# Kernel optimization log

Measured on AMD Instinct MI355X. Metric: run time of the kernel, lower is better.

Reference implementation:

```python
import jax, jax.numpy as jnp
import numpy as np

NUM_ENT = 50000
DIM = 128
NUM_REL = 1000  # num_rel * 2 (inverse relations)
E = 300000
SLOPE = 0.2      # args.leaky_relu_w
BN_EPS = 1e-5


def _leaky(x):
    return jax.nn.leaky_relu(x, SLOPE)


def _l2norm(x):
    n = jnp.linalg.norm(x, axis=-1, keepdims=True)
    return x / jnp.maximum(n, 1e-12)


def _batchnorm(x):
    # BatchNorm1d, training mode, fresh gamma=1/beta=0
    m = x.mean(axis=0)
    v = x.var(axis=0)
    return (x - m) / jnp.sqrt(v + BN_EPS)


def _propagate(i, j, etype, rel, x, watt, aatt, gcn, norm, num_ent):
    # gather -> relation-aware transform (opn='mult') -> attention -> scatter-add
    trans = x[j] * rel[etype]                       # [E, D]
    comb = jnp.concatenate([x[i], trans], axis=1)   # [E, 2D]
    score = (_leaky(comb @ watt) @ aatt)[:, 0]      # [E]
    # scatter softmax of attention score over destination nodes
    m = jax.ops.segment_max(score, i, num_segments=num_ent)
    m = jnp.where(jnp.isfinite(m), m, 0.0)
    e = jnp.exp(score - m[i])
    s = jax.ops.segment_sum(e, i, num_segments=num_ent)
    alpha = e / (s[i] + 1e-16)
    msg = (trans @ gcn) * alpha[:, None]
    if norm is not None:
        msg = msg * norm[:, None]
    return jax.ops.segment_sum(msg, i, num_segments=num_ent)


def _conv(ent, rel_in, edge_index, edge_type, w1, w2, gcn, loop_rel, watt, aatt):
    # RelationalAwareLayer.forward
    num_ent = ent.shape[0]
    rel = jnp.concatenate([rel_in, loop_rel], axis=0)
    rel = _leaky(rel @ w1) @ w2
    row, col = edge_index[0], edge_index[1]
    deg = jax.ops.segment_sum(jnp.ones((row.shape[0],), jnp.float32), row, num_segments=num_ent)
    dinv = jnp.where(deg > 0, deg ** -0.5, 0.0)
    norm = dinv[row]
    msg_n = _propagate(row, col, edge_type, rel, ent, watt, aatt, gcn, norm, num_ent)
    idx = jnp.arange(num_ent)
    loop_t = jnp.full((num_ent,), rel.shape[0] - 1)
    msg_s = _propagate(idx, idx, loop_t, rel, ent, watt, aatt, gcn, None, num_ent)
    return jnp.tanh(_batchnorm((msg_n + msg_s) / 2.0))


def setup_inputs() -> dict:
    key = jax.random.key(0)
    ks = jax.random.split(key, 24)
    g = lambda k, s: jax.random.normal(k, s, dtype=jnp.float32) * 0.05
    return {
        'edge_index': jax.random.randint(ks[0], (2, E), 0, NUM_ENT),
        'edge_type': jax.random.randint(ks[1], (E,), 0, NUM_REL),
        'ent_info_att': g(ks[2], (NUM_ENT, DIM)),
        'ent_completion_att': g(ks[3], (NUM_ENT, DIM)),
        'rel_completion_att': g(ks[4], (NUM_REL, DIM)),
        'rel_info_att': g(ks[5], (NUM_REL, DIM)),
        'align_linear1_1': g(ks[6], (2 * DIM, DIM)),
        'align_linear1_2': g(ks[7], (DIM, DIM)),
        'align_linear2_1': g(ks[8], (2 * DIM, DIM)),
        'align_linear2_2': g(ks[9], (DIM, DIM)),
        'rel_linear11': g(ks[10], (DIM, DIM)),
        'rel_linear12': g(ks[11], (DIM, DIM)),
        'rel_linear11_align': g(ks[12], (DIM, DIM)),
        'rel_linear12_align': g(ks[13], (DIM, DIM)),
        'all_linear_comp': g(ks[14], (3 * DIM, DIM)),
        # stacked per-layer conv params: [conv1_align, conv1_completion, conv2_align]
        'conv_w1': g(ks[15], (3, DIM, DIM)),
        'conv_w2': g(ks[16], (3, DIM, DIM)),
        'conv_gcn': g(ks[17], (3, DIM, DIM)),
        'conv_loop': g(ks[18], (3, 1, DIM)),
        'conv_watt': g(ks[19], (3, 2 * DIM, DIM)),
        'conv_aatt': g(ks[20], (3, DIM, 1)),
    }


def reference(edge_index, edge_type, ent_info_att, ent_completion_att,
              rel_completion_att, rel_info_att,
              align_linear1_1, align_linear1_2, align_linear2_1, align_linear2_2,
              rel_linear11, rel_linear12, rel_linear11_align, rel_linear12_align,
              all_linear_comp, conv_w1, conv_w2, conv_gcn, conv_loop, conv_watt, conv_aatt):
    # forward_base with num_gcn_layer == 2, dropout rate 0 (identity)
    init_comp = _l2norm(ent_completion_att)
    e1 = _leaky(jnp.concatenate([init_comp, ent_info_att], axis=1) @ align_linear1_1) @ align_linear1_2
    ao1 = _conv(e1, rel_info_att, edge_index, edge_type,
                conv_w1[0], conv_w2[0], conv_gcn[0], conv_loop[0], conv_watt[0], conv_aatt[0])
    co1 = _conv(ent_completion_att, rel_completion_att, edge_index, edge_type,
                conv_w1[1], conv_w2[1], conv_gcn[1], conv_loop[1], conv_watt[1], conv_aatt[1])
    pos1n = _l2norm(co1)
    e2 = _leaky(jnp.concatenate([pos1n, ao1], axis=1) @ align_linear2_1) @ align_linear2_2
    pr1 = _leaky(rel_completion_att @ rel_linear11) @ rel_linear12
    ari = _leaky(rel_info_att @ rel_linear11_align) @ rel_linear12_align
    ao2 = _conv(e2, ari, edge_index, edge_type,
                conv_w1[2], conv_w2[2], conv_gcn[2], conv_loop[2], conv_watt[2], conv_aatt[2])
    out = jnp.concatenate([e1, ao1, ao2], axis=1) @ all_linear_comp
    return (out, co1, pr1)
```

## Files before the change

### kernel.cpp

```cpp
#include <hip/hip_runtime.h>
#include <hip/hip_bf16.h>
#include <math.h>

#define D 128
#define DD 16384
#define NEMAX 96
typedef unsigned short u16;
typedef __attribute__((ext_vector_type(8))) short short8v;
typedef __attribute__((ext_vector_type(4))) short short4v;
typedef __attribute__((ext_vector_type(4))) float f32x4;

__device__ __forceinline__ u16 f2s(float v){
    union { __hip_bfloat16 h; u16 u; } c; c.h = __float2bfloat16(v); return c.u;
}
__device__ __forceinline__ float s2f(u16 u){
    union { __hip_bfloat16 h; u16 u; } c; c.u = u; return __bfloat162float(c.h);
}
__device__ __forceinline__ float lrelu(float x){ return x > 0.f ? x : 0.2f*x; }

__global__ void k_prepz(int* __restrict__ zz, int zw, int* __restrict__ nstart,
                        int* __restrict__ nend, int nb){
    int i = blockIdx.x*blockDim.x + threadIdx.x;
    int stride = gridDim.x*blockDim.x;
    for (int k = i; k < zw; k += stride) zz[k] = 0;
    for (int k = i; k < nb; k += stride){ nstart[k] = 0x7fffffff; nend[k] = -1; }
}
__global__ void k_f2b4(const float* __restrict__ in, u16* __restrict__ out, int n4){
    for (int i = blockIdx.x*blockDim.x + threadIdx.x; i < n4; i += gridDim.x*blockDim.x){
        float4 a = ((const float4*)in)[i];
        short4v pk;
        pk[0] = (short)f2s(a.x); pk[1] = (short)f2s(a.y);
        pk[2] = (short)f2s(a.z); pk[3] = (short)f2s(a.w);
        *(short4v*)(out + (size_t)i*4) = pk;
    }
}
__global__ void k_ideg(const int* __restrict__ row, int* __restrict__ deg, int E_){
    for (int i = blockIdx.x*blockDim.x + threadIdx.x; i < E_; i += gridDim.x*blockDim.x)
        atomicAdd(&deg[row[i]], 1);
}
__global__ void k_scan1(const int* __restrict__ ideg, int* __restrict__ rowptr,
                        int* __restrict__ bsum, int n){
    __shared__ int buf[256];
    int t = threadIdx.x, i = blockIdx.x*256 + t;
    int v = (i < n) ? ideg[i] : 0;
    buf[t] = v;
    __syncthreads();
    #pragma unroll
    for (int o = 1; o < 256; o <<= 1){
        int u = (t >= o) ? buf[t-o] : 0;
        __syncthreads();
        buf[t] += u;
        __syncthreads();
    }
    if (i < n) rowptr[i] = buf[t] - v;
    if (t == 255) bsum[blockIdx.x] = buf[255];
}
__global__ void k_scan2(int* __restrict__ bsum, int nb){
    __shared__ int buf[256];
    __shared__ int carry_s;
    int t = threadIdx.x;
    if (t == 0) carry_s = 0;
    __syncthreads();
    for (int base = 0; base < nb; base += 256){
        int v = (base + t < nb) ? bsum[base + t] : 0;
        buf[t] = v;
        __syncthreads();
        #pragma unroll
        for (int o = 1; o < 256; o <<= 1){
            int u = (t >= o) ? buf[t-o] : 0;
            __syncthreads();
            buf[t] += u;
            __syncthreads();
        }
        if (base + t < nb) bsum[base + t] = carry_s + buf[t] - v;
        int last = buf[255];
        __syncthreads();
        if (t == 0) carry_s += last;
        __syncthreads();
    }
}
__global__ void k_scan3(int* __restrict__ rowptr, const int* __restrict__ bsum,
                        const int* __restrict__ ideg, int* __restrict__ nstart,
                        int* __restrict__ nend, int n, int E_){
    int i = blockIdx.x*blockDim.x + threadIdx.x;
    if (i < n){
        int rpi = rowptr[i] + bsum[i >> 8];
        rowptr[i] = rpi;
        if (i == 0) rowptr[n] = E_;
        if (ideg[i] > 0){
            int b = rpi >> 6;
            atomicMin(&nstart[b], i);
            atomicMax(&nend[b], i);
        }
    }
}
__global__ void k_scatter(const int* __restrict__ row, const int* __restrict__ col,
                          const int* __restrict__ ety, const int* __restrict__ rowptr,
                          int* __restrict__ cnt, unsigned* __restrict__ jk, int E_){
    for (int e = blockIdx.x*blockDim.x + threadIdx.x; e < E_; e += gridDim.x*blockDim.x){
        int i = row[e];
        int pos = rowptr[i] + atomicAdd(&cnt[i], 1);
        jk[pos] = ((unsigned)col[e] & 0xFFFFu) | ((unsigned)ety[e] << 16);
    }
}
__global__ void k_bnapply(const u16* __restrict__ acc, const float* __restrict__ gp,
                          float inv_ne, int n, u16* __restrict__ dstb,
                          float* __restrict__ dstf){
    int d = threadIdx.x & 127;
    float m = gp[d] * inv_ne;
    float var = gp[128 + d] * inv_ne - m*m;
    float sc = rsqrtf(var + 1e-5f);
    for (int i = blockIdx.x*blockDim.x + threadIdx.x; i < n; i += gridDim.x*blockDim.x){
        float v = s2f(acc[i]) * 0.5f;
        float r = tanhf((v - m) * sc);
        dstb[i] = f2s(r);
        if (dstf) dstf[i] = r;
    }
}
__global__ void k_bnapply2(const u16* __restrict__ acc0, const float* __restrict__ gp0,
                           u16* __restrict__ d0b,
                           const u16* __restrict__ acc1, const float* __restrict__ gp1,
                           u16* __restrict__ d1b, float* __restrict__ d1f,
                           float inv_ne, int n, int gb){
    int pb = blockIdx.x >= gb;
    const u16* acc = pb ? acc1 : acc0;
    const float* gp = pb ? gp1 : gp0;
    u16* db = pb ? d1b : d0b;
    float* df = pb ? d1f : nullptr;
    int b = blockIdx.x - (pb ? gb : 0);
    int d = threadIdx.x & 127;
    float m = gp[d] * inv_ne;
    float var = gp[128 + d] * inv_ne - m*m;
    float sc = rsqrtf(var + 1e-5f);
    for (int i = b*blockDim.x + threadIdx.x; i < n; i += gb*blockDim.x){
        float v = s2f(acc[i]) * 0.5f;
        float r = tanhf((v - m) * sc);
        db[i] = f2s(r);
        if (df) df[i] = r;
    }
}

__global__ void k_relprep(const float* __restrict__ rel_comp, const float* __restrict__ rel_info,
        const float* __restrict__ rl11, const float* __restrict__ rl12,
        const float* __restrict__ rl11a, const float* __restrict__ rl12a,
        const float* __restrict__ cloop, const float* __restrict__ cw1,
        const float* __restrict__ cw2, float* __restrict__ pr1out,
        float* __restrict__ rel2all, int NR){
    int b = blockIdx.x, t = threadIdx.x;
    __shared__ float v[D];
    __shared__ float h[D];
    if (b < NR){
        v[t] = rel_comp[(size_t)b*D + t];
        __syncthreads();
        float a = 0.f;
        #pragma unroll 8
        for (int k = 0; k < D; k++) a += v[k] * rl11[(size_t)k*D + t];
        h[t] = lrelu(a);
        __syncthreads();
        float o = 0.f;
        #pragma unroll 8
        for (int k = 0; k < D; k++) o += h[k] * rl12[(size_t)k*D + t];
        pr1out[(size_t)b*D + t] = o;
        return;
    }
    int bb = b - NR;
    int l = bb / (NR+1), r = bb - l*(NR+1);
    float xv;
    if (r == NR)      xv = cloop[l*D + t];
    else if (l == 1)  xv = rel_comp[(size_t)r*D + t];
    else              xv = rel_info[(size_t)r*D + t];
    v[t] = xv;
    __syncthreads();
    if (l == 2 && r < NR){
        float a = 0.f;
        #pragma unroll 8
        for (int k = 0; k < D; k++) a += v[k] * rl11a[(size_t)k*D + t];
        h[t] = lrelu(a);
        __syncthreads();
        float o = 0.f;
        #pragma unroll 8
        for (int k = 0; k < D; k++) o += h[k] * rl12a[(size_t)k*D + t];
        v[t] = o;
        __syncthreads();
    }
    const float* w1 = cw1 + (size_t)l*DD;
    const float* w2 = cw2 + (size_t)l*DD;
    float a = 0.f;
    #pragma unroll 8
    for (int k = 0; k < D; k++) a += v[k] * w1[(size_t)k*D + t];
    h[t] = lrelu(a);
    __syncthreads();
    float o = 0.f;
    #pragma unroll 8
    for (int k = 0; k < D; k++) o += h[k] * w2[(size_t)k*D + t];
    rel2all[((size_t)l*(NR+1) + r)*D + t] = o;
}

struct TEnt { const float* s; u16* d; int ldd; };
struct TTab { TEnt e[18]; };
__global__ void k_wprep(TTab tab){
    TEnt en = tab.e[blockIdx.x];
    int t = threadIdx.x;
    int n = t >> 1, h = t & 1;
    #pragma unroll
    for (int g = 0; g < 8; ++g){
        int k0 = h*64 + g*8;
        short8v pk;
        #pragma unroll
        for (int q = 0; q < 8; ++q) pk[q] = (short)f2s(en.s[(size_t)(k0+q)*D + n]);
        *(short8v*)(en.d + (size_t)n*en.ldd + k0) = pk;
    }
}

struct Srcs { const void* p0; const void* p1; const void* p2; int f0, f1, f2; };

template<int NSEG, int EPI, bool RSN>
__global__ __launch_bounds__(256) void k_mrow(Srcs S, const u16* __restrict__ WT,
        void* __restrict__ out, int NE_){
    __shared__ __align__(16) short As[128*128];
    int tid = threadIdx.x;
    int row0 = blockIdx.x * 128;
    int lane = tid & 63, w = tid >> 6;
    int l15 = lane & 15, lq = lane >> 4;
    int nhalf = w & 1, mquad = w >> 1;
    f32x4 acc[4][4];
    #pragma unroll
    for (int a = 0; a < 4; a++)
        #pragma unroll
        for (int b = 0; b < 4; b++) acc[a][b] = (f32x4){0.f,0.f,0.f,0.f};

    int sr = tid >> 1, sh = tid & 1;
    int rr = row0 + sr; if (rr >= NE_) rr = NE_ - 1;

    #pragma unroll
    for (int s = 0; s < NSEG; ++s){
        const void* sp = (s == 0) ? S.p0 : (s == 1) ? S.p1 : S.p2;
        int sf = (s == 0) ? S.f0 : (s == 1) ? S.f1 : S.f2;
        if (s) __syncthreads();
        #pragma unroll
        for (int g = 0; g < 8; ++g){
            int k8 = sh*64 + g*8;
            short8v pk;
            if (sf){
                const float* fp = (const float*)sp + (size_t)rr*D + k8;
                #pragma unroll
                for (int q = 0; q < 8; ++q) pk[q] = (short)f2s(fp[q]);
            } else {
                pk = *(const short8v*)((const u16*)sp + (size_t)rr*D + k8);
            }
            *(short8v*)(As + sr*D + (((k8>>3) ^ (sr&7))<<3)) = pk;
        }
        if (RSN && s == 0){
            float ss = 0.f;
            #pragma unroll
            for (int g = 0; g < 8; ++g){
                int k8 = sh*64 + g*8;
                short8v v = *(const short8v*)(As + sr*D + (((k8>>3) ^ (sr&7))<<3));
                #pragma unroll
                for (int q = 0; q < 8; ++q){ float f = s2f((u16)v[q]); ss += f*f; }
            }
            ss += __shfl_xor(ss, 1, 64);
            float rsc = 1.f / fmaxf(sqrtf(ss), 1e-12f);
            #pragma unroll
            for (int g = 0; g < 8; ++g){
                int k8 = sh*64 + g*8;
                short* ap = As + sr*D + (((k8>>3) ^ (sr&7))<<3);
                short8v v = *(const short8v*)ap;
                short8v pk;
                #pragma unroll
                for (int q = 0; q < 8; ++q) pk[q] = (short)f2s(s2f((u16)v[q]) * rsc);
                *(short8v*)ap = pk;
            }
        }
        __syncthreads();
        short8v bfr[4][4];
        #pragma unroll
        for (int nt = 0; nt < 4; ++nt)
            #pragma unroll
            for (int kk = 0; kk < 4; ++kk){
                size_t idx = (size_t)(nhalf*64 + nt*16 + l15)*(NSEG*D) + (size_t)s*D + kk*32 + lq*8;
                bfr[nt][kk] = *(const short8v*)(WT + idx);
            }
        #pragma unroll
        for (int mt = 0; mt < 4; ++mt){
            int ar = mquad*64 + mt*16 + l15;
            short8v afr[4];
            #pragma unroll
            for (int kk = 0; kk < 4; ++kk)
                afr[kk] = *(const short8v*)(As + ar*D + (((kk*4 + lq) ^ (ar&7))<<3));
            #pragma unroll
            for (int nt = 0; nt < 4; ++nt)
                #pragma unroll
                for (int kk = 0; kk < 4; ++kk)
                    acc[mt][nt] = __builtin_amdgcn_mfma_f32_16x16x32_bf16(
                        afr[kk], bfr[nt][kk], acc[mt][nt], 0, 0, 0);
        }
    }
    #pragma unroll
    for (int mt = 0; mt < 4; ++mt){
        #pragma unroll
        for (int nt = 0; nt < 4; ++nt){
            #pragma unroll
            for (int r = 0; r < 4; ++r){
                int gr = row0 + mquad*64 + mt*16 + lq*4 + r;
                if (gr >= NE_) continue;
                int c = nhalf*64 + nt*16 + l15;
                float v = acc[mt][nt][r];
                if (EPI == 0) ((float*)out)[(size_t)gr*D + c] = v;
                else ((u16*)out)[(size_t)gr*D + c] = f2s(EPI == 2 ? lrelu(v) : v);
            }
        }
    }
}

struct ConvP { const u16* x; const u16* WT; u16* out; u16* ub; const float* loop; float* gp; };

template<int MODE>
__global__ __launch_bounds__(256) void k_mrow2(ConvP A, ConvP B, int rb, int NE_){
    __shared__ __align__(16) short As[128*128];
    int pb = blockIdx.x >= rb;
    ConvP P = pb ? B : A;
    int row0 = (blockIdx.x - (pb ? rb : 0)) * 128;
    int tid = threadIdx.x;
    int lane = tid & 63, w = tid >> 6;
    int l15 = lane & 15, lq = lane >> 4;
    int nhalf = w & 1, mquad = w >> 1;
    f32x4 acc[4][4];
    #pragma unroll
    for (int a = 0; a < 4; a++)
        #pragma unroll
        for (int b = 0; b < 4; b++) acc[a][b] = (f32x4){0.f,0.f,0.f,0.f};

    int sr = tid >> 1, sh = tid & 1;
    int rr = row0 + sr; if (rr >= NE_) rr = NE_ - 1;
    #pragma unroll
    for (int g = 0; g < 8; ++g){
        int k8 = sh*64 + g*8;
        short8v pk = *(const short8v*)(P.x + (size_t)rr*D + k8);
        *(short8v*)(As + sr*D + (((k8>>3) ^ (sr&7))<<3)) = pk;
    }
    __syncthreads();
    short8v bfr[4][4];
    #pragma unroll
    for (int nt = 0; nt < 4; ++nt)
        #pragma unroll
        for (int kk = 0; kk < 4; ++kk)
            bfr[nt][kk] = *(const short8v*)(P.WT + (size_t)(nhalf*64 + nt*16 + l15)*D + kk*32 + lq*8);
    #pragma unroll
    for (int mt = 0; mt < 4; ++mt){
        int ar = mquad*64 + mt*16 + l15;
        short8v afr[4];
        #pragma unroll
        for (int kk = 0; kk < 4; ++kk)
            afr[kk] = *(const short8v*)(As + ar*D + (((kk*4 + lq) ^ (ar&7))<<3));
        #pragma unroll
        for (int nt = 0; nt < 4; ++nt)
            #pragma unroll
            for (int kk = 0; kk < 4; ++kk)
                acc[mt][nt] = __builtin_amdgcn_mfma_f32_16x16x32_bf16(
                    afr[kk], bfr[nt][kk], acc[mt][nt], 0, 0, 0);
    }
    if (MODE == 3){
        float cs[4] = {0,0,0,0}, cs2[4] = {0,0,0,0};
        #pragma unroll
        for (int mt = 0; mt < 4; ++mt)
            #pragma unroll
            for (int nt = 0; nt < 4; ++nt)
                #pragma unroll
                for (int r = 0; r < 4; ++r){
                    int gr = row0 + mquad*64 + mt*16 + lq*4 + r;
                    if (gr >= NE_) continue;
                    int c = nhalf*64 + nt*16 + l15;
                    float v = acc[mt][nt][r];
                    P.out[(size_t)gr*D + c] = f2s(v);
                    float h = v * 0.5f;
                    cs[nt] += h; cs2[nt] += h*h;
                }
        __syncthreads();
        float* ps  = (float*)As;
        float* ps2 = ps + 1024;
        int slot = mquad*4 + lq;
        #pragma unroll
        for (int nt = 0; nt < 4; ++nt){
            int c = nhalf*64 + nt*16 + l15;
            ps[slot*128 + c]  = cs[nt];
            ps2[slot*128 + c] = cs2[nt];
        }
        __syncthreads();
        if (tid < 128){
            float s = 0.f, s2 = 0.f;
            #pragma unroll
            for (int q = 0; q < 8; ++q){ s += ps[q*128 + tid]; s2 += ps2[q*128 + tid]; }
            atomicAdd(&P.gp[tid], s);
            atomicAdd(&P.gp[128 + tid], s2);
        }
    } else {
        #pragma unroll
        for (int mt = 0; mt < 4; ++mt)
            #pragma unroll
            for (int nt = 0; nt < 4; ++nt)
                #pragma unroll
                for (int r = 0; r < 4; ++r){
                    int gr = row0 + mquad*64 + mt*16 + lq*4 + r;
                    if (gr >= NE_) continue;
                    int c = nhalf*64 + nt*16 + l15;
                    P.out[(size_t)gr*D + c] = f2s(acc[mt][nt][r]);
                }
        for (int idx = tid; idx < 128*128; idx += 256){
            int r2 = idx >> 7, c = idx & 127;
            int gr = row0 + r2;
            if (gr < NE_){
                float v = s2f((u16)As[r2*D + ((((c>>3) ^ (r2&7))<<3) | (c&7))]) * P.loop[c];
                P.ub[(size_t)gr*D + c] = f2s(v);
            }
        }
    }
}

struct FP { const u16* x; const float* rel2; const u16* xattb; const u16* WT;
            const float* aatt; const float* loop; u16* u; };

__global__ __launch_bounds__(256) void k_fedge(
        const unsigned* __restrict__ jk,
        const int* __restrict__ rowptr,
        const int* __restrict__ nstart, const int* __restrict__ nend,
        FP fa, FP fb, int nb){
    __shared__ __align__(16) short As[NEMAX*D];
    __shared__ u16 jL[NEMAX], kL[NEMAX], iL[NEMAX];
    __shared__ float sc[NEMAX];
    __shared__ float red[2][NEMAX];
    int pb = blockIdx.x >= nb;
    FP P = pb ? fb : fa;
    int b = blockIdx.x - (pb ? nb : 0);
    int ns = nstart[b];
    if (ns == 0x7fffffff) return;
    int nn = nend[b] - ns + 1;
    int tid = threadIdx.x;
    int estart = rowptr[ns];
    int ne = rowptr[ns + nn] - estart;
    if (ne > NEMAX) ne = NEMAX;
    int T = (ne + 15) >> 4;
    int nrows = T << 4;
    if (tid < ne){
        unsigned v = jk[estart + tid];
        jL[tid] = (u16)(v & 0xFFFFu); kL[tid] = (u16)(v >> 16);
    }
    if (tid < nn){
        int i = ns + tid;
        int s0 = rowptr[i] - estart, s1 = rowptr[i+1] - estart;
        if (s0 < 0) s0 = 0;
        if (s1 > NEMAX) s1 = NEMAX;
        for (int p = s0; p < s1; ++p) iL[p] = (u16)i;
    }
    __syncthreads();
    for (int it = tid; it < nrows*4; it += 256){
        int p = it >> 2, part = it & 3;
        int ps = (p < ne) ? p : (ne - 1);
        int j = jL[ps], krel = kL[ps];
        #pragma unroll
        for (int g = 0; g < 4; ++g){
            int k8 = part*32 + g*8;
            short8v sv = *(const short8v*)(P.x + (size_t)j*D + k8);
            const float* rp = P.rel2 + (size_t)krel*D + k8;
            short8v pk;
            #pragma unroll
            for (int q = 0; q < 8; ++q) pk[q] = (short)f2s(s2f((u16)sv[q]) * rp[q]);
            *(short8v*)(As + p*D + (((k8>>3) ^ (p&7))<<3)) = pk;
        }
    }
    __syncthreads();
    int lane = tid & 63, w = tid >> 6;
    int l15 = lane & 15, lq = lane >> 4;
    int nhalf = w & 1, mq = w >> 1;
    short8v bfr[4][4];
    #pragma unroll
    for (int nt = 0; nt < 4; ++nt)
        #pragma unroll
        for (int kk = 0; kk < 4; ++kk)
            bfr[nt][kk] = *(const short8v*)(P.WT + (size_t)(nhalf*64 + nt*16 + l15)*D + kk*32 + lq*8);
    float av[4];
    #pragma unroll
    for (int nt = 0; nt < 4; ++nt) av[nt] = P.aatt[nhalf*64 + nt*16 + l15];

    for (int t = mq; t < T; t += 2){
        float xv[4][4];
        #pragma unroll
        for (int r = 0; r < 4; ++r){
            int el = t*16 + lq*4 + r;
            int ep = (el < ne) ? el : (ne - 1);
            int ii = iL[ep];
            #pragma unroll
            for (int nt = 0; nt < 4; ++nt)
                xv[r][nt] = s2f(P.xattb[(size_t)ii*D + nhalf*64 + nt*16 + l15]);
        }
        int ar = t*16 + l15;
        short8v afr[4];
        #pragma unroll
        for (int kk = 0; kk < 4; ++kk)
            afr[kk] = *(const short8v*)(As + ar*D + (((kk*4 + lq) ^ (ar&7))<<3));
        f32x4 acc[4];
        #pragma unroll
        for (int nt = 0; nt < 4; ++nt) acc[nt] = (f32x4){0.f,0.f,0.f,0.f};
        #pragma unroll
        for (int nt = 0; nt < 4; ++nt)
            #pragma unroll
            for (int kk = 0; kk < 4; ++kk)
                acc[nt] = __builtin_amdgcn_mfma_f32_16x16x32_bf16(
                    afr[kk], bfr[nt][kk], acc[nt], 0, 0, 0);
        #pragma unroll
        for (int r = 0; r < 4; ++r){
            int el = t*16 + lq*4 + r;
            float p = 0.f;
            if (el < ne){
                #pragma unroll
                for (int nt = 0; nt < 4; ++nt)
                    p += lrelu(acc[nt][r] + xv[r][nt]) * av[nt];
            }
            p += __shfl_xor(p, 1, 64);
            p += __shfl_xor(p, 2, 64);
            p += __shfl_xor(p, 4, 64);
            p += __shfl_xor(p, 8, 64);
            if (l15 == 0 && el < NEMAX) red[nhalf][el] = p;
        }
    }
    __syncthreads();
    if (tid < ne) sc[tid] = expf(red[0][tid] + red[1][tid]);
    __syncthreads();
    if (tid < nn){
        int i = ns + tid;
        int s0 = rowptr[i] - estart, s1 = rowptr[i+1] - estart;
        if (s1 > NEMAX) s1 = NEMAX;
        if (s1 > s0){
            float sum = 0.f;
            for (int p = s0; p < s1; ++p) sum += sc[p];
            float coef = rsqrtf((float)(s1 - s0)) / (sum + 1e-16f);
            for (int p = s0; p < s1; ++p) sc[p] *= coef;
        }
    }
    __syncthreads();
    int c = tid & 127, nh = tid >> 7;
    float loopc = P.loop[c];
    for (int n = nh; n < nn; n += 2){
        int i = ns + n;
        int s0 = rowptr[i] - estart, s1 = rowptr[i+1] - estart;
        if (s1 > NEMAX) s1 = NEMAX;
        if (s1 <= s0) continue;
        float a = s2f(P.x[(size_t)i*D + c]) * loopc;
        int p = s0;
        for (; p + 4 <= s1; p += 4){
            float v0 = s2f((u16)As[(p+0)*D + ((((c>>3) ^ ((p+0)&7))<<3) | (c&7))]);
            float v1 = s2f((u16)As[(p+1)*D + ((((c>>3) ^ ((p+1)&7))<<3) | (c&7))]);
            float v2 = s2f((u16)As[(p+2)*D + ((((c>>3) ^ ((p+2)&7))<<3) | (c&7))]);
            float v3 = s2f((u16)As[(p+3)*D + ((((c>>3) ^ ((p+3)&7))<<3) | (c&7))]);
            a += sc[p]*v0 + sc[p+1]*v1 + sc[p+2]*v2 + sc[p+3]*v3;
        }
        for (; p < s1; ++p)
            a += sc[p] * s2f((u16)As[p*D + ((((c>>3) ^ (p&7))<<3) | (c&7))]);
        P.u[(size_t)i*D + c] = f2s(a);
    }
}

extern "C" void kernel_launch(void* const* d_in, const int* in_sizes, int n_in,
                              void* d_out, int out_size, void* d_ws, size_t ws_size,
                              hipStream_t stream){
    const int* eidx = (const int*)d_in[0];
    const int* ety  = (const int*)d_in[1];
    const float* ent_info = (const float*)d_in[2];
    const float* ent_comp = (const float*)d_in[3];
    const float* rel_comp = (const float*)d_in[4];
    const float* rel_info = (const float*)d_in[5];
    const float* al11 = (const float*)d_in[6],  *al12 = (const float*)d_in[7];
    const float* al21 = (const float*)d_in[8],  *al22 = (const float*)d_in[9];
    const float* rl11 = (const float*)d_in[10], *rl12 = (const float*)d_in[11];
    const float* rl11a = (const float*)d_in[12], *rl12a = (const float*)d_in[13];
    const float* allw = (const float*)d_in[14];
    const float* cw1 = (const float*)d_in[15], *cw2 = (const float*)d_in[16];
    const float* cgcn = (const float*)d_in[17], *cloop = (const float*)d_in[18];
    const float* cwatt = (const float*)d_in[19], *caatt = (const float*)d_in[20];

    const int E  = in_sizes[1];
    const int NE = in_sizes[2] / D;
    const int NR = in_sizes[4] / D;
    const int* row = eidx;
    const int* col = eidx + E;
    const size_t NEd = (size_t)NE * D;
    float* outp = (float*)d_out;
    const int NB64 = (E + 63) / 64;

    char* wsb = (char*)d_ws;
    size_t off = 0;
    auto takeB = [&](size_t bytes) -> void* {
        void* q = wsb + off;
        off = (off + bytes + 255) & ~(size_t)255;
        return q;
    };
    u16*   slotA = (u16*) takeB(NEd * 2);
    u16*   hb    = slotA;
    u16*   accB0 = slotA;
    u16*   xattb0= (u16*) takeB(NEd * 2);
    u16*   ub0   = (u16*) takeB(NEd * 2);
    u16*   e1b   = (u16*) takeB(NEd * 2);
    u16*   ao1b  = (u16*) takeB(NEd * 2);
    u16*   e2b   = (u16*) takeB(NEd * 2);
    u16*   cob   = (u16*) takeB(NEd * 2);
    float* rel2all = (float*)takeB((size_t)3*(NR+1)*D*4);
    int*   rowptr= (int*)  takeB((size_t)(NE+1)*4);
    unsigned* jk = (unsigned*)takeB((size_t)E*4);
    int*   bsum  = (int*)  takeB(1024*4);
    int*   nstart= (int*)  takeB((size_t)NB64*4);
    int*   nend  = (int*)  takeB((size_t)NB64*4);
    int ZW = 2*NE + 768;
    int*   zz    = (int*)  takeB((size_t)ZW*4);
    int*   ideg  = zz;
    int*   cnt   = zz + NE;
    float* gp3   = (float*)(zz + 2*NE);
    u16*   wtXatt = (u16*)takeB((size_t)3*DD*2);
    u16*   wtScore= (u16*)takeB((size_t)3*DD*2);
    u16*   wtGcn  = (u16*)takeB((size_t)3*DD*2);
    u16*   wtAl11 = (u16*)takeB((size_t)2*DD*2);
    u16*   wtAl12 = (u16*)takeB((size_t)DD*2);
    u16*   wtAl21 = (u16*)takeB((size_t)2*DD*2);
    u16*   wtAl22 = (u16*)takeB((size_t)DD*2);
    u16*   wtAllw = (u16*)takeB((size_t)3*DD*2);
    u16*   xcb   = e2b;

    size_t slab = ((NEd*2 + 255) & ~(size_t)255);
    bool wide = (off + 3*slab) <= ws_size;
    u16* xattb1 = wide ? (u16*)takeB(NEd * 2) : xattb0;
    u16* ub1    = wide ? (u16*)takeB(NEd * 2) : ub0;
    u16* accB1  = wide ? (u16*)takeB(NEd * 2) : accB0;

    const int GS = 2048, BS = 256;
    const int RB = (NE + 127) / 128;
    const int NB = (NE + 255) / 256;
    const float inv_ne = 1.f / (float)NE;

    TTab tab;
    int ti = 0;
    for (int l = 0; l < 3; ++l){
        tab.e[ti++] = { cwatt + (size_t)l*2*DD,        wtXatt  + (size_t)l*DD, 128 };
        tab.e[ti++] = { cwatt + (size_t)l*2*DD + DD,   wtScore + (size_t)l*DD, 128 };
        tab.e[ti++] = { cgcn  + (size_t)l*DD,          wtGcn   + (size_t)l*DD, 128 };
    }
    tab.e[ti++] = { al11,       wtAl11,        256 };
    tab.e[ti++] = { al11 + DD,  wtAl11 + 128,  256 };
    tab.e[ti++] = { al12,       wtAl12,        128 };
    tab.e[ti++] = { al21,       wtAl21,        256 };
    tab.e[ti++] = { al21 + DD,  wtAl21 + 128,  256 };
    tab.e[ti++] = { al22,       wtAl22,        128 };
    tab.e[ti++] = { allw,            wtAllw,        384 };
    tab.e[ti++] = { allw + DD,       wtAllw + 128,  384 };
    tab.e[ti++] = { allw + 2*DD,     wtAllw + 256,  384 };
    k_wprep<<<18, 256, 0, stream>>>(tab);

    k_prepz<<<256, BS, 0, stream>>>(zz, ZW, nstart, nend, NB64);
    k_f2b4<<<GS, BS, 0, stream>>>(ent_comp, xcb, (int)(NEd/4));
    k_ideg<<<GS, BS, 0, stream>>>(row, ideg, E);
    k_scan1<<<NB, 256, 0, stream>>>(ideg, rowptr, bsum, NE);
    k_scan2<<<1, 256, 0, stream>>>(bsum, NB);
    k_scan3<<<NB, 256, 0, stream>>>(rowptr, bsum, ideg, nstart, nend, NE, E);
    k_scatter<<<GS, BS, 0, stream>>>(row, col, ety, rowptr, cnt, jk, E);

    k_relprep<<<NR + 3*(NR+1), D, 0, stream>>>(rel_comp, rel_info, rl11, rl12,
                                               rl11a, rl12a, cloop, cw1, cw2,
                                               outp + 2*NEd, rel2all, NR);

    {
        Srcs S{ ent_comp, ent_info, nullptr, 1, 1, 0 };
        k_mrow<2, 2, true><<<RB, 256, 0, stream>>>(S, wtAl11, hb, NE);
        Srcs S2{ hb, nullptr, nullptr, 0, 0, 0 };
        k_mrow<1, 1, false><<<RB, 256, 0, stream>>>(S2, wtAl12, e1b, NE);
    }

    auto conv_seq = [&](const u16* x, int l, u16* xab, u16* ubp, u16* acb,
                        u16* dstb, float* dstf){
        const float* rel2l = rel2all + (size_t)l*(NR+1)*D;
        float* gp = gp3 + (size_t)l*256;
        ConvP A4{ x, wtXatt + (size_t)l*DD, xab, ubp, rel2l + (size_t)NR*D, nullptr };
        k_mrow2<4><<<RB, 256, 0, stream>>>(A4, A4, RB, NE);
        FP fa{ x, rel2l, xab, wtScore + (size_t)l*DD, caatt + (size_t)l*D,
               rel2l + (size_t)NR*D, ubp };
        k_fedge<<<NB64, 256, 0, stream>>>(jk, rowptr, nstart, nend, fa, fa, NB64);
        ConvP A3{ ubp, wtGcn + (size_t)l*DD, acb, nullptr, nullptr, gp };
        k_mrow2<3><<<RB, 256, 0, stream>>>(A3, A3, RB, NE);
        k_bnapply<<<GS, BS, 0, stream>>>(acb, gp, inv_ne, (int)NEd, dstb, dstf);
    };

    if (wide){
        const float* rel2_0 = rel2all;
        const float* rel2_1 = rel2all + (size_t)(NR+1)*D;
        ConvP A4{ e1b, wtXatt,      xattb0, ub0, rel2_0 + (size_t)NR*D, nullptr };
        ConvP B4{ xcb, wtXatt + DD, xattb1, ub1, rel2_1 + (size_t)NR*D, nullptr };
        k_mrow2<4><<<2*RB, 256, 0, stream>>>(A4, B4, RB, NE);
        FP fa{ e1b, rel2_0, xattb0, wtScore,      caatt,     rel2_0 + (size_t)NR*D, ub0 };
        FP fb{ xcb, rel2_1, xattb1, wtScore + DD, caatt + D, rel2_1 + (size_t)NR*D, ub1 };
        k_fedge<<<2*NB64, 256, 0, stream>>>(jk, rowptr, nstart, nend, fa, fb, NB64);
        ConvP A3{ ub0, wtGcn,      accB0, nullptr, nullptr, gp3 };
        ConvP B3{ ub1, wtGcn + DD, accB1, nullptr, nullptr, gp3 + 256 };
        k_mrow2<3><<<2*RB, 256, 0, stream>>>(A3, B3, RB, NE);
        k_bnapply2<<<2*GS, BS, 0, stream>>>(accB0, gp3, ao1b,
                                            accB1, gp3 + 256, cob, outp + NEd,
                                            inv_ne, (int)NEd, GS);
    } else {
        conv_seq(e1b, 0, xattb0, ub0, accB0, ao1b, nullptr);
        conv_seq(xcb, 1, xattb0, ub0, accB0, cob, outp + NEd);
    }

    {
        Srcs S{ cob, ao1b, nullptr, 0, 0, 0 };
        k_mrow<2, 2, true><<<RB, 256, 0, stream>>>(S, wtAl21, hb, NE);
        Srcs S2{ hb, nullptr, nullptr, 0, 0, 0 };
        k_mrow<1, 1, false><<<RB, 256, 0, stream>>>(S2, wtAl22, e2b, NE);
    }

    conv_seq(e2b, 2, xattb0, ub0, accB0, cob, nullptr);

    {
        Srcs S{ e1b, ao1b, cob, 0, 0, 0 };
        k_mrow<3, 0, false><<<RB, 256, 0, stream>>>(S, wtAllw, outp, NE);
    }
}
```

Before: 664.4 us.

## Fold self-loop term into GCN GEMM via concatenated K=256 weight

Removes the self-loop vector x*loop that was written to the ub buffer in the xatt GEMM and used to seed the per-node accumulation in the edge kernel. The GCN GEMM now runs with K=256 over [ub, x] against a precomputed weight that concatenates W and diag(loop)*W. This drops the extra ub write and x reads in the first two kernels, at the cost of a second A-tile load and double the MFMA work in the GCN GEMM. It also adds kernels to zero ub, because nodes with no edges are no longer written, and rounding changes since loop*W is stored in bf16.

```diff
diff --git a/kernel.cpp b/kernel.cpp
--- a/kernel.cpp
+++ b/kernel.cpp
@@ -24,6 +24,10 @@
     int stride = gridDim.x*blockDim.x;
     for (int k = i; k < zw; k += stride) zz[k] = 0;
     for (int k = i; k < nb; k += stride){ nstart[k] = 0x7fffffff; nend[k] = -1; }
+}
+__global__ void k_zeroi(int* __restrict__ p, int n){
+    for (int i = blockIdx.x*blockDim.x + threadIdx.x; i < n; i += gridDim.x*blockDim.x)
+        p[i] = 0;
 }
 __global__ void k_f2b4(const float* __restrict__ in, u16* __restrict__ out, int n4){
     for (int i = blockIdx.x*blockDim.x + threadIdx.x; i < n4; i += gridDim.x*blockDim.x){
@@ -211,6 +215,19 @@
         *(short8v*)(en.d + (size_t)n*en.ldd + k0) = pk;
     }
 }
+__global__ void k_wgl(const u16* __restrict__ wtGcn, const float* __restrict__ rel2all,
+                      int NR, u16* __restrict__ wtGcnC){
+    int l = blockIdx.x, t = threadIdx.x;
+    const u16* src = wtGcn + (size_t)l*DD;
+    const float* loop = rel2all + ((size_t)l*(NR+1) + NR)*D;
+    u16* dst = wtGcnC + (size_t)l*2*DD;
+    for (int idx = t; idx < DD; idx += 256){
+        int n = idx >> 7, k = idx & 127;
+        u16 w = src[idx];
+        dst[(size_t)n*256 + k] = w;
+        dst[(size_t)n*256 + 128 + k] = f2s(s2f(w) * loop[k]);
+    }
+}
 
 struct Srcs { const void* p0; const void* p1; const void* p2; int f0, f1, f2; };
 
@@ -313,13 +330,12 @@
     }
 }
 
-struct ConvP { const u16* x; const u16* WT; u16* out; u16* ub; const float* loop; float* gp; };
-
-template<int MODE>
-__global__ __launch_bounds__(256) void k_mrow2(ConvP A, ConvP B, int rb, int NE_){
+struct XP { const u16* x; const u16* WT; u16* out; };
+
+__global__ __launch_bounds__(256) void k_xatt2(XP A, XP B, int rb, int NE_){
     __shared__ __align__(16) short As[128*128];
     int pb = blockIdx.x >= rb;
-    ConvP P = pb ? B : A;
+    XP P = pb ? B : A;
     int row0 = (blockIdx.x - (pb ? rb : 0)) * 128;
     int tid = threadIdx.x;
     int lane = tid & 63, w = tid >> 6;
@@ -330,7 +346,6 @@
     for (int a = 0; a < 4; a++)
         #pragma unroll
         for (int b = 0; b < 4; b++) acc[a][b] = (f32x4){0.f,0.f,0.f,0.f};
-
     int sr = tid >> 1, sh = tid & 1;
     int rr = row0 + sr; if (rr >= NE_) rr = NE_ - 1;
     #pragma unroll
@@ -360,65 +375,108 @@
                 acc[mt][nt] = __builtin_amdgcn_mfma_f32_16x16x32_bf16(
                     afr[kk], bfr[nt][kk], acc[mt][nt], 0, 0, 0);
     }
-    if (MODE == 3){
-        float cs[4] = {0,0,0,0}, cs2[4] = {0,0,0,0};
-        #pragma unroll
-        for (int mt = 0; mt < 4; ++mt)
+    #pragma unroll
+    for (int mt = 0; mt < 4; ++mt)
+        #pragma unroll
+        for (int nt = 0; nt < 4; ++nt)
+            #pragma unroll
+            for (int r = 0; r < 4; ++r){
+                int gr = row0 + mquad*64 + mt*16 + lq*4 + r;
+                if (gr >= NE_) continue;
+                int c = nhalf*64 + nt*16 + l15;
+                P.out[(size_t)gr*D + c] = f2s(acc[mt][nt][r]);
+            }
+}
+
+struct GP { const u16* ub; const u16* x; const u16* WT; u16* out; float* gp; };
+
+__global__ __launch_bounds__(256) void k_gcn2(GP A, GP B, int rb, int NE_){
+    __shared__ __align__(16) short As[128*128];
+    int pb = blockIdx.x >= rb;
+    GP P = pb ? B : A;
+    int row0 = (blockIdx.x - (pb ? rb : 0)) * 128;
+    int tid = threadIdx.x;
+    int lane = tid & 63, w = tid >> 6;
+    int l15 = lane & 15, lq = lane >> 4;
+    int nhalf = w & 1, mquad = w >> 1;
+    f32x4 acc[4][4];
+    #pragma unroll
+    for (int a = 0; a < 4; a++)
+        #pragma unroll
+        for (int b = 0; b < 4; b++) acc[a][b] = (f32x4){0.f,0.f,0.f,0.f};
+    int sr = tid >> 1, sh = tid & 1;
+    int rr = row0 + sr; if (rr >= NE_) rr = NE_ - 1;
+    #pragma unroll
+    for (int s = 0; s < 2; ++s){
+        const u16* sp = s ? P.x : P.ub;
+        if (s) __syncthreads();
+        #pragma unroll
+        for (int g = 0; g < 8; ++g){
+            int k8 = sh*64 + g*8;
+            short8v pk = *(const short8v*)(sp + (size_t)rr*D + k8);
+            *(short8v*)(As + sr*D + (((k8>>3) ^ (sr&7))<<3)) = pk;
+        }
+        __syncthreads();
+        short8v bfr[4][4];
+        #pragma unroll
+        for (int nt = 0; nt < 4; ++nt)
+            #pragma unroll
+            for (int kk = 0; kk < 4; ++kk){
+                size_t idx = (size_t)(nhalf*64 + nt*16 + l15)*256 + (size_t)s*D + kk*32 + lq*8;
+                bfr[nt][kk] = *(const short8v*)(P.WT + idx);
+            }
+        #pragma unroll
+        for (int mt = 0; mt < 4; ++mt){
+            int ar = mquad*64 + mt*16 + l15;
+            short8v afr[4];
+            #pragma unroll
+            for (int kk = 0; kk < 4; ++kk)
+                afr[kk] = *(const short8v*)(As + ar*D + (((kk*4 + lq) ^ (ar&7))<<3));
             #pragma unroll
             for (int nt = 0; nt < 4; ++nt)
                 #pragma unroll
-                for (int r = 0; r < 4; ++r){
-                    int gr = row0 + mquad*64 + mt*16 + lq*4 + r;
-                    if (gr >= NE_) continue;
-                    int c = nhalf*64 + nt*16 + l15;
-                    float v = acc[mt][nt][r];
-                    P.out[(size_t)gr*D + c] = f2s(v);
-                    float h = v * 0.5f;
-                    cs[nt] += h; cs2[nt] += h*h;
-                }
-        __syncthreads();
-        float* ps  = (float*)As;
-        float* ps2 = ps + 1024;
-        int slot = mquad*4 + lq;
-        #pragma unroll
-        for (int nt = 0; nt < 4; ++nt){
-            int c = nhalf*64 + nt*16 + l15;
-            ps[slot*128 + c]  = cs[nt];
-            ps2[slot*128 + c] = cs2[nt];
-        }
-        __syncthreads();
-        if (tid < 128){
-            float s = 0.f, s2 = 0.f;
-            #pragma unroll
-            for (int q = 0; q < 8; ++q){ s += ps[q*128 + tid]; s2 += ps2[q*128 + tid]; }
-            atomicAdd(&P.gp[tid], s);
-            atomicAdd(&P.gp[128 + tid], s2);
-        }
-    } else {
-        #pragma unroll
-        for (int mt = 0; mt < 4; ++mt)
-            #pragma unroll
-            for (int nt = 0; nt < 4; ++nt)
-                #pragma unroll
-                for (int r = 0; r < 4; ++r){
-                    int gr = row0 + mquad*64 + mt*16 + lq*4 + r;
-                    if (gr >= NE_) continue;
-                    int c = nhalf*64 + nt*16 + l15;
-                    P.out[(size_t)gr*D + c] = f2s(acc[mt][nt][r]);
-                }
-        for (int idx = tid; idx < 128*128; idx += 256){
-            int r2 = idx >> 7, c = idx & 127;
-            int gr = row0 + r2;
-            if (gr < NE_){
-                float v = s2f((u16)As[r2*D + ((((c>>3) ^ (r2&7))<<3) | (c&7))]) * P.loop[c];
-                P.ub[(size_t)gr*D + c] = f2s(v);
-            }
-        }
+                for (int kk = 0; kk < 4; ++kk)
+                    acc[mt][nt] = __builtin_amdgcn_mfma_f32_16x16x32_bf16(
+                        afr[kk], bfr[nt][kk], acc[mt][nt], 0, 0, 0);
+        }
+    }
+    float cs[4] = {0,0,0,0}, cs2[4] = {0,0,0,0};
+    #pragma unroll
+    for (int mt = 0; mt < 4; ++mt)
+        #pragma unroll
+        for (int nt = 0; nt < 4; ++nt)
+            #pragma unroll
+            for (int r = 0; r < 4; ++r){
+                int gr = row0 + mquad*64 + mt*16 + lq*4 + r;
+                if (gr >= NE_) continue;
+                int c = nhalf*64 + nt*16 + l15;
+                float v = acc[mt][nt][r];
+                P.out[(size_t)gr*D + c] = f2s(v);
+                float h = v * 0.5f;
+                cs[nt] += h; cs2[nt] += h*h;
+            }
+    __syncthreads();
+    float* ps  = (float*)As;
+    float* ps2 = ps + 1024;
+    int slot = mquad*4 + lq;
+    #pragma unroll
+    for (int nt = 0; nt < 4; ++nt){
+        int c = nhalf*64 + nt*16 + l15;
+        ps[slot*128 + c]  = cs[nt];
+        ps2[slot*128 + c] = cs2[nt];
+    }
+    __syncthreads();
+    if (tid < 128){
+        float s = 0.f, s2 = 0.f;
+        #pragma unroll
+        for (int q = 0; q < 8; ++q){ s += ps[q*128 + tid]; s2 += ps2[q*128 + tid]; }
+        atomicAdd(&P.gp[tid], s);
+        atomicAdd(&P.gp[128 + tid], s2);
     }
 }
 
 struct FP { const u16* x; const float* rel2; const u16* xattb; const u16* WT;
-            const float* aatt; const float* loop; u16* u; };
+            const float* aatt; u16* u; };
 
 __global__ __launch_bounds__(256) void k_fedge(
         const unsigned* __restrict__ jk,
@@ -539,13 +597,12 @@
     }
     __syncthreads();
     int c = tid & 127, nh = tid >> 7;
-    float loopc = P.loop[c];
     for (int n = nh; n < nn; n += 2){
         int i = ns + n;
         int s0 = rowptr[i] - estart, s1 = rowptr[i+1] - estart;
         if (s1 > NEMAX) s1 = NEMAX;
         if (s1 <= s0) continue;
-        float a = s2f(P.x[(size_t)i*D + c]) * loopc;
+        float a = 0.f;
         int p = s0;
         for (; p + 4 <= s1; p += 4){
             float v0 = s2f((u16)As[(p+0)*D + ((((c>>3) ^ ((p+0)&7))<<3) | (c&7))]);
@@ -617,6 +674,7 @@
     u16*   wtXatt = (u16*)takeB((size_t)3*DD*2);
     u16*   wtScore= (u16*)takeB((size_t)3*DD*2);
     u16*   wtGcn  = (u16*)takeB((size_t)3*DD*2);
+    u16*   wtGcnC = (u16*)takeB((size_t)3*2*DD*2);
     u16*   wtAl11 = (u16*)takeB((size_t)2*DD*2);
     u16*   wtAl12 = (u16*)takeB((size_t)DD*2);
     u16*   wtAl21 = (u16*)takeB((size_t)2*DD*2);
@@ -654,6 +712,8 @@
     k_wprep<<<18, 256, 0, stream>>>(tab);
 
     k_prepz<<<256, BS, 0, stream>>>(zz, ZW, nstart, nend, NB64);
+    k_zeroi<<<256, BS, 0, stream>>>((int*)ub0, (int)(NEd/2));
+    if (wide) k_zeroi<<<256, BS, 0, stream>>>((int*)ub1, (int)(NEd/2));
     k_f2b4<<<GS, BS, 0, stream>>>(ent_comp, xcb, (int)(NEd/4));
     k_ideg<<<GS, BS, 0, stream>>>(row, ideg, E);
     k_scan1<<<NB, 256, 0, stream>>>(ideg, rowptr, bsum, NE);
@@ -664,6 +724,7 @@
     k_relprep<<<NR + 3*(NR+1), D, 0, stream>>>(rel_comp, rel_info, rl11, rl12,
                                                rl11a, rl12a, cloop, cw1, cw2,
                                                outp + 2*NEd, rel2all, NR);
+    k_wgl<<<3, 256, 0, stream>>>(wtGcn, rel2all, NR, wtGcnC);
 
     {
         Srcs S{ ent_comp, ent_info, nullptr, 1, 1, 0 };
@@ -676,28 +737,27 @@
                         u16* dstb, float* dstf){
         const float* rel2l = rel2all + (size_t)l*(NR+1)*D;
         float* gp = gp3 + (size_t)l*256;
-        ConvP A4{ x, wtXatt + (size_t)l*DD, xab, ubp, rel2l + (size_t)NR*D, nullptr };
-        k_mrow2<4><<<RB, 256, 0, stream>>>(A4, A4, RB, NE);
-        FP fa{ x, rel2l, xab, wtScore + (size_t)l*DD, caatt + (size_t)l*D,
-               rel2l + (size_t)NR*D, ubp };
+        XP X{ x, wtXatt + (size_t)l*DD, xab };
+        k_xatt2<<<RB, 256, 0, stream>>>(X, X, RB, NE);
+        FP fa{ x, rel2l, xab, wtScore + (size_t)l*DD, caatt + (size_t)l*D, ubp };
         k_fedge<<<NB64, 256, 0, stream>>>(jk, rowptr, nstart, nend, fa, fa, NB64);
-        ConvP A3{ ubp, wtGcn + (size_t)l*DD, acb, nullptr, nullptr, gp };
-        k_mrow2<3><<<RB, 256, 0, stream>>>(A3, A3, RB, NE);
+        GP G{ ubp, x, wtGcnC + (size_t)l*2*DD, acb, gp };
+        k_gcn2<<<RB, 256, 0, stream>>>(G, G, RB, NE);
         k_bnapply<<<GS, BS, 0, stream>>>(acb, gp, inv_ne, (int)NEd, dstb, dstf);
     };
 
     if (wide){
         const float* rel2_0 = rel2all;
         const float* rel2_1 = rel2all + (size_t)(NR+1)*D;
-        ConvP A4{ e1b, wtXatt,      xattb0, ub0, rel2_0 + (size_t)NR*D, nullptr };
-        ConvP B4{ xcb, wtXatt + DD, xattb1, ub1, rel2_1 + (size_t)NR*D, nullptr };
-        k_mrow2<4><<<2*RB, 256, 0, stream>>>(A4, B4, RB, NE);
-        FP fa{ e1b, rel2_0, xattb0, wtScore,      caatt,     rel2_0 + (size_t)NR*D, ub0 };
-        FP fb{ xcb, rel2_1, xattb1, wtScore + DD, caatt + D, rel2_1 + (size_t)NR*D, ub1 };
+        XP XA{ e1b, wtXatt,      xattb0 };
+        XP XB{ xcb, wtXatt + DD, xattb1 };
+        k_xatt2<<<2*RB, 256, 0, stream>>>(XA, XB, RB, NE);
+        FP fa{ e1b, rel2_0, xattb0, wtScore,      caatt,     ub0 };
+        FP fb{ xcb, rel2_1, xattb1, wtScore + DD, caatt + D, ub1 };
         k_fedge<<<2*NB64, 256, 0, stream>>>(jk, rowptr, nstart, nend, fa, fb, NB64);
-        ConvP A3{ ub0, wtGcn,      accB0, nullptr, nullptr, gp3 };
-        ConvP B3{ ub1, wtGcn + DD, accB1, nullptr, nullptr, gp3 + 256 };
-        k_mrow2<3><<<2*RB, 256, 0, stream>>>(A3, B3, RB, NE);
+        GP GA{ ub0, e1b, wtGcnC,          accB0, gp3 };
+        GP GB{ ub1, xcb, wtGcnC + 2*DD,   accB1, gp3 + 256 };
+        k_gcn2<<<2*RB, 256, 0, stream>>>(GA, GB, RB, NE);
         k_bnapply2<<<2*GS, BS, 0, stream>>>(accB0, gp3, ao1b,
                                             accB1, gp3 + 256, cob, outp + NEd,
                                             inv_ne, (int)NEd, GS);
```

Measured after the change: 634.1 us. 4.6% less time.
